# Performance work log

Measured on AMD Instinct MI355X. Metric: run time of the kernel, lower is better.

Reference implementation:

```python
import jax, jax.numpy as jnp
import numpy as np
from jax import lax

S = 2048      # num_states
V = 32768     # num_observations
T = 4096      # sequence length


def setup_inputs() -> dict:
    key = jax.random.key(0)
    k_obs, k_a, k_b, k_pi = jax.random.split(key, 4)
    observations = jax.random.randint(k_obs, (T,), 0, V)
    # A: row-stochastic so the unnormalized alpha recursion stays finite over T steps.
    A = jax.random.uniform(k_a, (S, S), dtype=jnp.float32)
    A = A / jnp.sum(A, axis=1, keepdims=True)
    # B: emission factors near 1 to avoid exponential under/overflow.
    B = jax.random.uniform(k_b, (S, V), dtype=jnp.float32, minval=0.9, maxval=1.1)
    pi = jax.random.uniform(k_pi, (S,), dtype=jnp.float32)
    return {"observations": observations, "A": A, "B": B, "pi": pi}


def reference(observations, A, B, pi):
    # Gather emission columns once: [T, S]
    B_obs = B[:, observations].T
    alpha0 = pi * B_obs[0]  # [S]

    def step(alpha, b_t):
        # alpha_t = (alpha_{t-1} @ A) * B[:, obs_t]
        alpha_new = jnp.matmul(alpha, A) * b_t
        return alpha_new, None

    alpha_T, _ = lax.scan(step, alpha0, B_obs[1:])
    return jnp.sum(alpha_T)
```

## Files before the change

### kernel.cpp

```cpp
#include <hip/hip_runtime.h>


#define S 2048
#define V 32768
#define T 4096
#define G 128
#define BT 512
#define COLS 16
#define RING 16
#define DIST 8

#define SM_AS    0
#define SM_AL    32768
#define SM_BR    (32768 + 544 * 4)
#define SM_WP    (SM_BR + RING * COLS)
#define SM_FP    (SM_WP + 8 * COLS)
#define SMEM_FLOATS (SM_FP + 8)
#define SMEM_BYTES  (SMEM_FLOATS * 4)

__global__ __launch_bounds__(BT, 1) void hmm_fwd(
    const int* __restrict__ obs,
    const float* __restrict__ A,
    const float* __restrict__ B,
    const float* __restrict__ pi,
    float* __restrict__ out,
    unsigned long long* __restrict__ buf)
{
    extern __shared__ float smem[];
    float4* As4    = (float4*)(smem + SM_AS);
    float4* al4    = (float4*)(smem + SM_AL);
    float*  bring  = smem + SM_BR;
    float*  wpart  = smem + SM_WP;
    float*  fpart  = smem + SM_FP;

    const int g    = blockIdx.x;
    const int tid  = threadIdx.x;
    const int lane = tid & 63;
    const int wave = tid >> 6;
    const int c    = tid & 15;
    const int rg   = tid >> 4;
    const int j    = g * COLS + c;

    {
        const int u  = tid & 3;
        const int r0 = tid >> 2;
        for (int it = 0; it < 16; ++it) {
            int r = r0 + 128 * it;
            float4 av = *(const float4*)(A + (size_t)r * S + g * COLS + 4 * u);
            float* dst = smem + SM_AS + ((r >> 2) * 16) * 4 + (r & 3);
            dst[(4 * u + 0) * 4] = av.x;
            dst[(4 * u + 1) * 4] = av.y;
            dst[(4 * u + 2) * 4] = av.z;
            dst[(4 * u + 3) * 4] = av.w;
        }
    }

    if (wave == 1 && lane < COLS) {
        int jj = g * COLS + lane;
        for (int u = 1; u <= DIST; ++u) {
            int o = obs[u];
            bring[(u & (RING - 1)) * COLS + lane] = B[(size_t)jj * V + o];
        }
    }
    if (wave == 0 && lane < COLS) {
        int o0 = obs[0];
        float v = pi[j] * B[(size_t)j * V + o0];
        unsigned long long p = (1ull << 32) | (unsigned long long)__float_as_uint(v);
        __hip_atomic_store(&buf[j], p, __ATOMIC_RELAXED, __HIP_MEMORY_SCOPE_AGENT);
    }

    __syncthreads();

    for (int t = 1; t < T; ++t) {
        float4 af[16];
#pragma unroll
        for (int k = 0; k < 16; ++k) af[k] = As4[(rg * 16 + k) * 16 + c];
#pragma unroll
        for (int k = 0; k < 16; ++k)
            asm volatile("" : "+v"(af[k].x), "+v"(af[k].y),
                              "+v"(af[k].z), "+v"(af[k].w));

        unsigned long long want = (unsigned long long)t;
        unsigned long long* src = buf + (((t - 1) & 1) * S) + 4 * tid;
        unsigned long long v0, v1, v2, v3;
        for (;;) {
            v0 = __hip_atomic_load(&src[0], __ATOMIC_RELAXED, __HIP_MEMORY_SCOPE_AGENT);
            v1 = __hip_atomic_load(&src[1], __ATOMIC_RELAXED, __HIP_MEMORY_SCOPE_AGENT);
            v2 = __hip_atomic_load(&src[2], __ATOMIC_RELAXED, __HIP_MEMORY_SCOPE_AGENT);
            v3 = __hip_atomic_load(&src[3], __ATOMIC_RELAXED, __HIP_MEMORY_SCOPE_AGENT);
            if ((v0 >> 32) == want && (v1 >> 32) == want &&
                (v2 >> 32) == want && (v3 >> 32) == want) break;
            __builtin_amdgcn_s_sleep(1);
        }
        float4 f;
        f.x = __uint_as_float((unsigned)v0);
        f.y = __uint_as_float((unsigned)v1);
        f.z = __uint_as_float((unsigned)v2);
        f.w = __uint_as_float((unsigned)v3);
        al4[tid + (tid >> 4)] = f;
        __syncthreads();

        if (wave == 1 && lane < COLS) {
            int tp = t + DIST;
            if (tp < T) {
                int o = obs[tp];
                bring[(tp & (RING - 1)) * COLS + lane] =
                    B[(size_t)(g * COLS + lane) * V + o];
            }
        }

        float acc_a = 0.f, acc_b = 0.f;
#pragma unroll
        for (int k = 0; k < 16; ++k) {
            int p = rg * 16 + k;
            float4 al = al4[p + (p >> 4)];
            if (k & 1) {
                acc_b = fmaf(al.x, af[k].x, acc_b);
                acc_b = fmaf(al.y, af[k].y, acc_b);
                acc_b = fmaf(al.z, af[k].z, acc_b);
                acc_b = fmaf(al.w, af[k].w, acc_b);
            } else {
                acc_a = fmaf(al.x, af[k].x, acc_a);
                acc_a = fmaf(al.y, af[k].y, acc_a);
                acc_a = fmaf(al.z, af[k].z, acc_a);
                acc_a = fmaf(al.w, af[k].w, acc_a);
            }
        }
        float acc = acc_a + acc_b;
        acc += __shfl_down(acc, 32, 64);
        acc += __shfl_down(acc, 16, 64);
        if (lane < 16) wpart[wave * 16 + lane] = acc;
        __syncthreads();

        if (wave == 0 && lane < 16) {
            float s = 0.f;
#pragma unroll
            for (int w = 0; w < 8; ++w) s += wpart[w * 16 + lane];
            float val = s * bring[(t & (RING - 1)) * COLS + lane];
            unsigned long long p = (((unsigned long long)(t + 1)) << 32) |
                                   (unsigned long long)__float_as_uint(val);
            __hip_atomic_store(&buf[(t & 1) * S + g * COLS + lane], p,
                               __ATOMIC_RELAXED, __HIP_MEMORY_SCOPE_AGENT);
        }
    }

    if (g == 0) {
        unsigned long long want = (unsigned long long)T;
        unsigned long long* src = buf + (((T - 1) & 1) * S) + 4 * tid;
        unsigned long long v0, v1, v2, v3;
        for (;;) {
            v0 = __hip_atomic_load(&src[0], __ATOMIC_RELAXED, __HIP_MEMORY_SCOPE_AGENT);
            v1 = __hip_atomic_load(&src[1], __ATOMIC_RELAXED, __HIP_MEMORY_SCOPE_AGENT);
            v2 = __hip_atomic_load(&src[2], __ATOMIC_RELAXED, __HIP_MEMORY_SCOPE_AGENT);
            v3 = __hip_atomic_load(&src[3], __ATOMIC_RELAXED, __HIP_MEMORY_SCOPE_AGENT);
            if ((v0 >> 32) == want && (v1 >> 32) == want &&
                (v2 >> 32) == want && (v3 >> 32) == want) break;
            __builtin_amdgcn_s_sleep(1);
        }
        float sm = __uint_as_float((unsigned)v0) + __uint_as_float((unsigned)v1) +
                   __uint_as_float((unsigned)v2) + __uint_as_float((unsigned)v3);
        sm += __shfl_down(sm, 32, 64);
        sm += __shfl_down(sm, 16, 64);
        sm += __shfl_down(sm, 8, 64);
        sm += __shfl_down(sm, 4, 64);
        sm += __shfl_down(sm, 2, 64);
        sm += __shfl_down(sm, 1, 64);
        if (lane == 0) fpart[wave] = sm;
        __syncthreads();
        if (tid == 0) {
            float tot = 0.f;
            for (int w = 0; w < 8; ++w) tot += fpart[w];
            out[0] = tot;
        }
    }
}

extern "C" void kernel_launch(void* const* d_in, const int* in_sizes, int n_in,
                              void* d_out, int out_size, void* d_ws, size_t ws_size,
                              hipStream_t stream) {
    const int*   obs = (const int*)d_in[0];
    const float* A   = (const float*)d_in[1];
    const float* B   = (const float*)d_in[2];
    const float* pi  = (const float*)d_in[3];
    float* out = (float*)d_out;
    unsigned long long* buf = (unsigned long long*)d_ws;

    hipFuncSetAttribute((const void*)hmm_fwd,
                        hipFuncAttributeMaxDynamicSharedMemorySize, SMEM_BYTES);


    void* args[] = { (void*)&obs, (void*)&A, (void*)&B, (void*)&pi,
                     (void*)&out, (void*)&buf };
    hipLaunchCooperativeKernel((void*)hmm_fwd, dim3(G), dim3(BT), args,
                               SMEM_BYTES, stream);
}
```

Before: 9.715 ms.

## Remap threads to 4 columns by 16 rows with swizzled A tile

```diff
diff --git a/kernel.cpp b/kernel.cpp
--- a/kernel.cpp
+++ b/kernel.cpp
@@ -12,7 +12,7 @@
 
 #define SM_AS    0
 #define SM_AL    32768
-#define SM_BR    (32768 + 544 * 4)
+#define SM_BR    (SM_AL + 2560)
 #define SM_WP    (SM_BR + RING * COLS)
 #define SM_FP    (SM_WP + 8 * COLS)
 #define SMEM_FLOATS (SM_FP + 8)
@@ -37,9 +37,8 @@
     const int tid  = threadIdx.x;
     const int lane = tid & 63;
     const int wave = tid >> 6;
-    const int c    = tid & 15;
-    const int rg   = tid >> 4;
-    const int j    = g * COLS + c;
+    const int cq   = tid & 3;
+    const int rg   = tid >> 2;
 
     {
         const int u  = tid & 3;
@@ -47,11 +46,7 @@
         for (int it = 0; it < 16; ++it) {
             int r = r0 + 128 * it;
             float4 av = *(const float4*)(A + (size_t)r * S + g * COLS + 4 * u);
-            float* dst = smem + SM_AS + ((r >> 2) * 16) * 4 + (r & 3);
-            dst[(4 * u + 0) * 4] = av.x;
-            dst[(4 * u + 1) * 4] = av.y;
-            dst[(4 * u + 2) * 4] = av.z;
-            dst[(4 * u + 3) * 4] = av.w;
+            As4[(r * 4 + u) ^ ((r >> 4) & 7)] = av;
         }
     }
 
@@ -63,10 +58,11 @@
         }
     }
     if (wave == 0 && lane < COLS) {
+        int jl = g * COLS + lane;
         int o0 = obs[0];
-        float v = pi[j] * B[(size_t)j * V + o0];
+        float v = pi[jl] * B[(size_t)jl * V + o0];
         unsigned long long p = (1ull << 32) | (unsigned long long)__float_as_uint(v);
-        __hip_atomic_store(&buf[j], p, __ATOMIC_RELAXED, __HIP_MEMORY_SCOPE_AGENT);
+        __hip_atomic_store(&buf[jl], p, __ATOMIC_RELAXED, __HIP_MEMORY_SCOPE_AGENT);
     }
 
     __syncthreads();
@@ -74,11 +70,12 @@
     for (int t = 1; t < T; ++t) {
         float4 af[16];
 #pragma unroll
-        for (int k = 0; k < 16; ++k) af[k] = As4[(rg * 16 + k) * 16 + c];
-#pragma unroll
-        for (int k = 0; k < 16; ++k)
-            asm volatile("" : "+v"(af[k].x), "+v"(af[k].y),
-                              "+v"(af[k].z), "+v"(af[k].w));
+        for (int r = 0; r < 16; ++r)
+            af[r] = As4[((rg * 16 + r) * 4 + cq) ^ (rg & 7)];
+#pragma unroll
+        for (int r = 0; r < 16; ++r)
+            asm volatile("" : "+v"(af[r].x), "+v"(af[r].y),
+                              "+v"(af[r].z), "+v"(af[r].w));
 
         unsigned long long want = (unsigned long long)t;
         unsigned long long* src = buf + (((t - 1) & 1) * S) + 4 * tid;
@@ -97,7 +94,7 @@
         f.y = __uint_as_float((unsigned)v1);
         f.z = __uint_as_float((unsigned)v2);
         f.w = __uint_as_float((unsigned)v3);
-        al4[tid + (tid >> 4)] = f;
+        al4[tid + (tid >> 2)] = f;
         __syncthreads();
 
         if (wave == 1 && lane < COLS) {
@@ -109,27 +106,41 @@
             }
         }
 
-        float acc_a = 0.f, acc_b = 0.f;
-#pragma unroll
-        for (int k = 0; k < 16; ++k) {
-            int p = rg * 16 + k;
-            float4 al = al4[p + (p >> 4)];
-            if (k & 1) {
-                acc_b = fmaf(al.x, af[k].x, acc_b);
-                acc_b = fmaf(al.y, af[k].y, acc_b);
-                acc_b = fmaf(al.z, af[k].z, acc_b);
-                acc_b = fmaf(al.w, af[k].w, acc_b);
-            } else {
-                acc_a = fmaf(al.x, af[k].x, acc_a);
-                acc_a = fmaf(al.y, af[k].y, acc_a);
-                acc_a = fmaf(al.z, af[k].z, acc_a);
-                acc_a = fmaf(al.w, af[k].w, acc_a);
-            }
-        }
-        float acc = acc_a + acc_b;
-        acc += __shfl_down(acc, 32, 64);
-        acc += __shfl_down(acc, 16, 64);
-        if (lane < 16) wpart[wave * 16 + lane] = acc;
+        float4 acc = {0.f, 0.f, 0.f, 0.f};
+#pragma unroll
+        for (int k = 0; k < 4; ++k) {
+            int p = rg * 4 + k;
+            float4 al = al4[p + (p >> 2)];
+            float4 a0 = af[4 * k + 0];
+            float4 a1 = af[4 * k + 1];
+            float4 a2 = af[4 * k + 2];
+            float4 a3 = af[4 * k + 3];
+            acc.x = fmaf(al.x, a0.x, acc.x);
+            acc.x = fmaf(al.y, a1.x, acc.x);
+            acc.x = fmaf(al.z, a2.x, acc.x);
+            acc.x = fmaf(al.w, a3.x, acc.x);
+            acc.y = fmaf(al.x, a0.y, acc.y);
+            acc.y = fmaf(al.y, a1.y, acc.y);
+            acc.y = fmaf(al.z, a2.y, acc.y);
+            acc.y = fmaf(al.w, a3.y, acc.y);
+            acc.z = fmaf(al.x, a0.z, acc.z);
+            acc.z = fmaf(al.y, a1.z, acc.z);
+            acc.z = fmaf(al.z, a2.z, acc.z);
+            acc.z = fmaf(al.w, a3.z, acc.z);
+            acc.w = fmaf(al.x, a0.w, acc.w);
+            acc.w = fmaf(al.y, a1.w, acc.w);
+            acc.w = fmaf(al.z, a2.w, acc.w);
+            acc.w = fmaf(al.w, a3.w, acc.w);
+        }
+#pragma unroll
+        for (int off = 32; off >= 4; off >>= 1) {
+            acc.x += __shfl_down(acc.x, off, 64);
+            acc.y += __shfl_down(acc.y, off, 64);
+            acc.z += __shfl_down(acc.z, off, 64);
+            acc.w += __shfl_down(acc.w, off, 64);
+        }
+        if (lane < 4)
+            *(float4*)(wpart + wave * 16 + lane * 4) = acc;
         __syncthreads();
 
         if (wave == 0 && lane < 16) {
```

After: 9.296 ms. -4.3%, faster.
